# Kernel optimization log

Measured on AMD Instinct MI355X. Metric: run time of the kernel, lower is better.

Reference implementation:

```python
import jax, jax.numpy as jnp
import numpy as np

# ---- problem sizes (would come from edge_index / init args in the torch module) ----
N = 10000      # number of nodes
E = 100000     # number of edges
C = 6          # channels per node
L = 6          # layers
B = 16         # batch
N_IN = 100     # input nodes  (nodes [0, N_IN))
N_OUT = 100    # output nodes (nodes [N-N_OUT, N))
EPS = 1e-5


def setup_inputs() -> dict:
    rng = np.random.default_rng(0)
    src = rng.integers(0, N, size=E).astype(np.int32)
    dst = rng.integers(0, N, size=E).astype(np.int32)

    input_mask = np.zeros(N, bool); input_mask[:N_IN] = True
    output_mask = np.zeros(N, bool); output_mask[N - N_OUT:] = True
    func_mask = ~(input_mask | output_mask)
    func_nodes = np.nonzero(func_mask)[0].astype(np.int32)
    F = func_nodes.size
    ii = np.arange(C, dtype=np.int32)

    # W1 (E -> C*N): edge e feeds all C channels of its dst node. nnz = E*C
    w1_rows = np.repeat(np.arange(E, dtype=np.int32), C)
    w1_cols = (dst[:, None] * C + ii[None, :]).reshape(-1)

    # W2 (C*N -> C*N): dense CxC block per function node. nnz = F*C*C
    base = np.repeat(func_nodes * C, C * C)
    w2_rows = base + np.tile(np.repeat(ii, C), F)
    w2_cols = base + np.tile(np.tile(ii, C), F)

    # W3 (C*N -> E): edge e reads the C channels of src(e) if src is a function node
    e_sel = np.nonzero(func_mask[src])[0].astype(np.int32)
    w3_rows = (src[e_sel][:, None] * C + ii[None, :]).reshape(-1)
    w3_cols = np.repeat(e_sel, C)

    # values: kaiming-style init with fan d (d=C for W1/W2, d=1 for W3)
    w1_vals = (rng.standard_normal(w1_rows.size) / np.sqrt(C)).astype(np.float32)
    w2_vals = (rng.standard_normal(w2_rows.size) / np.sqrt(C)).astype(np.float32)
    w3_vals = (rng.standard_normal(w3_rows.size) * 1.0).astype(np.float32)

    key = jax.random.key(0)
    x = jax.random.normal(key, (B, N), dtype=jnp.float32)

    return {
        "x": x,
        "src": jnp.asarray(src), "dst": jnp.asarray(dst),
        "output_mask": jnp.asarray(output_mask),
        "w1_rows": jnp.asarray(w1_rows), "w1_cols": jnp.asarray(w1_cols),
        "w1_vals": jnp.asarray(w1_vals), "b1": jnp.zeros((C * N,), jnp.float32),
        "w2_rows": jnp.asarray(w2_rows), "w2_cols": jnp.asarray(w2_cols),
        "w2_vals": jnp.asarray(w2_vals), "b2": jnp.zeros((C * N,), jnp.float32),
        "w3_rows": jnp.asarray(w3_rows), "w3_cols": jnp.asarray(w3_cols),
        "w3_vals": jnp.asarray(w3_vals), "b3": jnp.zeros((E,), jnp.float32),
        "gamma": jnp.ones((L,), jnp.float32), "beta": jnp.zeros((L,), jnp.float32),
    }


def _sp_lin(h, rows, cols, vals, bias, out_dim):
    # out[b, c] = sum_{k: cols[k]==c} h[b, rows[k]] * vals[k] + bias[c]
    contrib = h[:, rows] * vals  # [B, nnz]
    out = jnp.zeros((h.shape[0], out_dim), h.dtype).at[:, cols].add(contrib)
    return out + bias


def _batchnorm_scalar(z, g, b):
    # BatchNorm1d(1) on z.view(-1,1): single channel over all B*E elements (training mode)
    m = jnp.mean(z)
    v = jnp.mean(jnp.square(z - m))
    return (z - m) * jax.lax.rsqrt(v + EPS) * g + b


def reference(x, src, dst, output_mask,
              w1_rows, w1_cols, w1_vals, b1,
              w2_rows, w2_cols, w2_vals, b2,
              w3_rows, w3_cols, w3_vals, b3,
              gamma, beta):
    x0 = x[:, src]          # node2edge: [B, E]
    h = x0
    h_last = x0             # residual=True path
    for l in range(L):
        z = _sp_lin(h, w1_rows, w1_cols, w1_vals, b1, C * N)
        z = jax.nn.elu(z)
        z = _sp_lin(z, w2_rows, w2_cols, w2_vals, b2, C * N)
        z = jax.nn.elu(z)
        z = _sp_lin(z, w3_rows, w3_cols, w3_vals, b3, E)
        z = _batchnorm_scalar(z, gamma[l], beta[l])
        h = z + h_last
        h_last = h
    h = h / L
    # edge2node: scatter edge values to dst nodes, keep only output nodes
    node = jnp.zeros((x.shape[0], N), x.dtype).at[:, dst].add(h)
    return jnp.where(output_mask[None, :], node, 0.0)
```

## Files before the change

### kernel.cpp

```cpp
#include <hip/hip_runtime.h>
#include <math.h>

#define NN 10000
#define NE 100000
#define CC 6
#define LL 6
#define BB 16
#define FUNC_LO 100
#define FUNC_HI 9900
#define EPSF 1e-5f
#define NSLOT 64

struct Slot { double s1, s2; double pad[6]; };

struct Params {
  const float *x, *w1v, *b1, *w2v, *b2, *w3v, *b3, *gamma, *beta;
  const int *src, *dst, *w3r, *w3c;
  float *out;
  int *row_start, *counts, *fill, *slot;
  int *row2, *counts2, *fill2, *csr2;
  float4 *grec;
  float4 *srec;
  float *xT, *h, *z3a, *z3b;
  Slot *part, *baseS;
  int F, Ksel;
};

__device__ __forceinline__ float eluf(float x){ return x > 0.0f ? x : expm1f(x); }

__device__ void block_add_slot(double a, double q, Slot* sl){
  __shared__ double sb1[4], sb2[4];
  #pragma unroll
  for(int off=32;off;off>>=1){ a+=__shfl_down(a,off); q+=__shfl_down(q,off); }
  int wid = threadIdx.x>>6;
  if((threadIdx.x&63)==0){ sb1[wid]=a; sb2[wid]=q; }
  __syncthreads();
  if(threadIdx.x==0){
    double A=sb1[0]+sb1[1]+sb1[2]+sb1[3];
    double Q=sb2[0]+sb2[1]+sb2[2]+sb2[3];
    if(A!=0.0) atomicAdd(&sl->s1,A);
    if(Q!=0.0) atomicAdd(&sl->s2,Q);
  }
  __syncthreads();
}

__device__ void bn_params(const Slot* part, const Slot* baseS, float* m, float* inv){
  __shared__ double s_mv[2];
  if(threadIdx.x < NSLOT){
    double a = part[threadIdx.x].s1 + baseS[threadIdx.x].s1;
    double q = part[threadIdx.x].s2 + baseS[threadIdx.x].s2;
    #pragma unroll
    for(int off=32;off;off>>=1){ a+=__shfl_down(a,off); q+=__shfl_down(q,off); }
    if(threadIdx.x==0){
      const double cnt = (double)NE*(double)BB;
      double md = a/cnt, vd = q/cnt - md*md;
      s_mv[0]=md; s_mv[1]=1.0/sqrt(vd+(double)EPSF);
    }
  }
  __syncthreads();
  *m=(float)s_mv[0]; *inv=(float)s_mv[1];
  __syncthreads();
}

__global__ __launch_bounds__(256) void kw_P1(Params p){
  int tid = blockIdx.x*256 + threadIdx.x, nt = gridDim.x*256;
  for(int i=tid;i<NN*BB;i+=nt){ int n=i>>4, b=i&15; p.xT[i]=p.x[b*NN+n]; }
  double a=0.0,q=0.0;
  for(int e=tid;e<NE;e+=nt){
    atomicAdd(&p.counts[p.dst[e]],1);
    int s=p.src[e];
    if(!(s>=FUNC_LO && s<FUNC_HI)){ double v=(double)p.b3[e]; a+=v; q+=v*v; }
  }
  for(int k=tid;k<p.Ksel;k+=nt){
    int s=p.w3r[k*CC]/CC;
    atomicAdd(&p.counts2[s-FUNC_LO],1);
  }
  block_add_slot(a*BB, q*BB, &p.baseS[blockIdx.x&(NSLOT-1)]);
}

__global__ __launch_bounds__(256) void kw_scan(Params p){
  __shared__ int s_scan[256];
  const int*  cin  = (blockIdx.x==0)? p.counts : p.counts2;
  int*        rout = (blockIdx.x==0)? p.row_start : p.row2;
  const int   nel  = (blockIdx.x==0)? NN : p.F;
  const int   CH   = (nel+255)/256;
  int t=threadIdx.x, base=t*CH, s=0;
  for(int k=0;k<CH;k++){ int i=base+k; if(i<nel) s+=cin[i]; }
  s_scan[t]=s; __syncthreads();
  for(int off=1;off<256;off<<=1){
    int v=(t>=off)?s_scan[t-off]:0; __syncthreads();
    s_scan[t]+=v; __syncthreads();
  }
  int run=s_scan[t]-s;
  for(int k=0;k<CH;k++){ int i=base+k; if(i<nel){ rout[i]=run; run+=cin[i]; } }
  if(t==255) rout[nel]=s_scan[255];
}

__global__ __launch_bounds__(256) void kw_fill(Params p){
  int tid = blockIdx.x*256 + threadIdx.x, nt = gridDim.x*256;
  for(int e=tid;e<NE;e+=nt){
    int n=p.dst[e];
    int pos=p.row_start[n]+atomicAdd(&p.fill[n],1);
    p.slot[e]=pos;
    const float* w=&p.w1v[e*CC];
    int s=p.src[e];
    float b3v=p.b3[e];
    p.grec[pos*2  ]=make_float4(w[0],w[1],w[2],w[3]);
    p.grec[pos*2+1]=make_float4(w[4],w[5],__int_as_float(s),b3v);
    if(!(s>=FUNC_LO && s<FUNC_HI)){
      float4 v4=make_float4(b3v,b3v,b3v,b3v);
      float4* za=(float4*)&p.z3a[pos*BB];
      float4* zb=(float4*)&p.z3b[pos*BB];
      #pragma unroll
      for(int i=0;i<4;i++){ za[i]=v4; zb[i]=v4; }
    }
  }
  for(int k=tid;k<p.Ksel;k+=nt){
    int fi=p.w3r[k*CC]/CC - FUNC_LO;
    int pos=p.row2[fi]+atomicAdd(&p.fill2[fi],1);
    p.csr2[pos]=k;
  }
}

template<int MODE>
__global__ __launch_bounds__(256) void kw_AB(Params p, int l,
    const float* __restrict__ z3p, float* __restrict__ z3c){
  int tid = blockIdx.x*256 + (int)threadIdx.x, nt = gridDim.x*256;
  float c1=0.f, c2=0.f;
  if(MODE>0){
    float m, inv;
    bn_params(p.part+(l-1)*NSLOT, p.baseS, &m, &inv);
    float g=p.gamma[l-1], be=p.beta[l-1];
    c1 = inv*g; c2 = be - m*c1;
  }
  const int FB2 = p.F*32;
  double a=0.0, q=0.0;
  for(int t=tid;t<FB2;t+=nt){
    int fi = t>>5;
    int u  = t&31, b = u&15, half = u>>4;
    int n  = FUNC_LO+fi;
    float acc[CC];
    #pragma unroll
    for(int i=0;i<CC;i++) acc[i]=0.f;
    int beg=p.row_start[n], end=p.row_start[n+1];
    int pp = beg + half;
    for(; pp+2<end; pp+=4){
      float4 ra0=p.grec[pp*2],     rb0=p.grec[pp*2+1];
      float4 ra1=p.grec[(pp+2)*2], rb1=p.grec[(pp+2)*2+1];
      float hv0, hv1;
      if(MODE==0){
        int s0=__float_as_int(rb0.z), s1=__float_as_int(rb1.z);
        hv0 = p.xT[s0*BB+b];
        hv1 = p.xT[s1*BB+b];
      } else {
        float zb0=z3p[pp*BB+b], zb1=z3p[(pp+2)*BB+b];
        float hb0, hb1;
        if(MODE==1){
          int s0=__float_as_int(rb0.z), s1=__float_as_int(rb1.z);
          hb0=p.xT[s0*BB+b]; hb1=p.xT[s1*BB+b];
        } else {
          hb0=p.h[pp*BB+b]; hb1=p.h[(pp+2)*BB+b];
        }
        hv0 = hb0 + zb0*c1 + c2;
        hv1 = hb1 + zb1*c1 + c2;
        p.h[pp*BB+b]=hv0; p.h[(pp+2)*BB+b]=hv1;
      }
      acc[0]+=hv0*ra0.x+hv1*ra1.x; acc[1]+=hv0*ra0.y+hv1*ra1.y;
      acc[2]+=hv0*ra0.z+hv1*ra1.z; acc[3]+=hv0*ra0.w+hv1*ra1.w;
      acc[4]+=hv0*rb0.x+hv1*rb1.x; acc[5]+=hv0*rb0.y+hv1*rb1.y;
    }
    if(pp<end){
      float4 ra0=p.grec[pp*2], rb0=p.grec[pp*2+1];
      float hv0;
      if(MODE==0){
        int s0=__float_as_int(rb0.z);
        hv0 = p.xT[s0*BB+b];
      } else {
        float zb0=z3p[pp*BB+b];
        float hb0;
        if(MODE==1){ int s0=__float_as_int(rb0.z); hb0=p.xT[s0*BB+b]; }
        else       { hb0=p.h[pp*BB+b]; }
        hv0 = hb0 + zb0*c1 + c2;
        p.h[pp*BB+b]=hv0;
      }
      acc[0]+=hv0*ra0.x; acc[1]+=hv0*ra0.y; acc[2]+=hv0*ra0.z;
      acc[3]+=hv0*ra0.w; acc[4]+=hv0*rb0.x; acc[5]+=hv0*rb0.y;
    }
    #pragma unroll
    for(int i=0;i<CC;i++){
      acc[i] += __shfl_xor(acc[i],16);
      acc[i]  = eluf(acc[i] + p.b1[n*CC+i]);
    }
    const float* W2=&p.w2v[fi*36];
    float z2[CC];
    #pragma unroll
    for(int jj=0;jj<CC;jj++){
      float o=p.b2[n*CC+jj];
      #pragma unroll
      for(int i=0;i<CC;i++) o+=acc[i]*W2[i*CC+jj];
      z2[jj]=eluf(o);
    }
    int bg2=p.row2[fi], en2=p.row2[fi+1];
    if(MODE==0){
      for(int sp=bg2+half;sp<en2;sp+=2){
        int k=p.csr2[sp];
        int e=p.w3c[k*CC];
        const float* w=&p.w3v[k*CC];
        float b3v=p.b3[e];
        int sl=p.slot[e];
        if(b==0){
          p.srec[sp*2  ]=make_float4(w[0],w[1],w[2],w[3]);
          p.srec[sp*2+1]=make_float4(w[4],w[5],__int_as_float(sl),b3v);
        }
        float o = b3v + z2[0]*w[0]+z2[1]*w[1]+z2[2]*w[2]
                      + z2[3]*w[3]+z2[4]*w[4]+z2[5]*w[5];
        z3c[sl*BB+b]=o;
        a+=o; q+=(double)o*o;
      }
    } else {
      for(int sp=bg2+half;sp<en2;sp+=2){
        float4 ra=p.srec[sp*2], rb=p.srec[sp*2+1];
        float o = rb.w + z2[0]*ra.x + z2[1]*ra.y + z2[2]*ra.z
                       + z2[3]*ra.w + z2[4]*rb.x + z2[5]*rb.y;
        int sl=__float_as_int(rb.z);
        z3c[sl*BB+b]=o;
        a+=o; q+=(double)o*o;
      }
    }
  }
  if(MODE>0){
    int outBeg = p.row_start[FUNC_HI];
    int tot = (p.row_start[NN]-outBeg)*BB;
    for(int u=tid; u<tot; u+=nt){
      int pp=outBeg+(u>>4); int bb=u&15;
      float zb=z3p[pp*BB+bb];
      float hb;
      if(MODE==1){
        float4 rb=p.grec[pp*2+1];
        int s=__float_as_int(rb.z);
        hb=p.xT[s*BB+bb];
      } else {
        hb=p.h[pp*BB+bb];
      }
      p.h[pp*BB+bb]=hb+zb*c1+c2;
    }
  }
  block_add_slot(a,q,&p.part[l*NSLOT+(blockIdx.x&(NSLOT-1))]);
}

__global__ __launch_bounds__(256) void kw_out(Params p, const float* __restrict__ z3p){
  int tid = blockIdx.x*256 + threadIdx.x, nt = gridDim.x*256;
  float m,inv;
  bn_params(p.part+(LL-1)*NSLOT, p.baseS, &m, &inv);
  float g=p.gamma[LL-1], be=p.beta[LL-1];
  float c1=inv*g, c2=be-m*c1;
  for(int idx=tid;idx<BB*NN;idx+=nt){
    int b=idx/NN, n=idx-b*NN;
    float acc=0.f;
    if(n>=FUNC_HI){
      int beg=p.row_start[n], end=p.row_start[n+1];
      for(int pp=beg;pp<end;++pp){
        acc += p.h[pp*BB+b] + z3p[pp*BB+b]*c1 + c2;
      }
      acc *= (1.0f/(float)LL);
    }
    p.out[idx]=acc;
  }
}

extern "C" void kernel_launch(void* const* d_in, const int* in_sizes, int n_in,
                              void* d_out, int out_size, void* d_ws, size_t ws_size,
                              hipStream_t stream){
  Params p;
  p.x    =(const float*)d_in[0];
  p.src  =(const int*)  d_in[1];
  p.dst  =(const int*)  d_in[2];
  p.w1v  =(const float*)d_in[6];
  p.b1   =(const float*)d_in[7];
  p.w2v  =(const float*)d_in[10];
  p.b2   =(const float*)d_in[11];
  p.w3r  =(const int*)  d_in[12];
  p.w3c  =(const int*)  d_in[13];
  p.w3v  =(const float*)d_in[14];
  p.b3   =(const float*)d_in[15];
  p.gamma=(const float*)d_in[16];
  p.beta =(const float*)d_in[17];
  p.out  =(float*)d_out;
  p.F    = in_sizes[8]/36;
  p.Ksel = in_sizes[12]/CC;

  char* ws=(char*)d_ws; size_t off=0;
  auto alloc=[&](size_t bytes)->char*{
    char* q=ws+off; off=(off+bytes+255)&~(size_t)255; return q;
  };
  p.row_start=(int*)   alloc((NN+1)*sizeof(int));
  p.row2     =(int*)   alloc((size_t)(p.F+1)*sizeof(int));
  p.slot     =(int*)   alloc(NE*sizeof(int));
  p.csr2     =(int*)   alloc(NE*sizeof(int));
  p.grec     =(float4*)alloc((size_t)NE*2*sizeof(float4));
  p.srec     =(float4*)alloc((size_t)NE*2*sizeof(float4));
  p.xT       =(float*) alloc((size_t)NN*BB*sizeof(float));
  p.h        =(float*) alloc((size_t)NE*BB*sizeof(float));
  p.z3a      =(float*) alloc((size_t)NE*BB*sizeof(float));
  p.z3b      =(float*) alloc((size_t)NE*BB*sizeof(float));
  p.counts   =(int*)  alloc(NN*sizeof(int));
  p.fill     =(int*)  alloc(NN*sizeof(int));
  p.counts2  =(int*)  alloc((size_t)p.F*sizeof(int));
  p.fill2    =(int*)  alloc((size_t)p.F*sizeof(int));
  p.part     =(Slot*) alloc((size_t)LL*NSLOT*sizeof(Slot));
  p.baseS    =(Slot*) alloc((size_t)NSLOT*sizeof(Slot));
  (void)ws_size; (void)n_in; (void)out_size;

  size_t zspan = (char*)(p.baseS+NSLOT) - (char*)p.counts;
  hipMemsetAsync(p.counts, 0, zspan, stream);

  float* bufs[2] = { p.z3a, p.z3b };
  const int gridAB = (p.F*32 + 255)/256;

  kw_P1  <<<512,256,0,stream>>>(p);
  kw_scan<<<2,  256,0,stream>>>(p);
  kw_fill<<<512,256,0,stream>>>(p);
  kw_AB<0><<<gridAB,256,0,stream>>>(p, 0, bufs[1], bufs[0]);
  kw_AB<1><<<gridAB,256,0,stream>>>(p, 1, bufs[0], bufs[1]);
  for(int l=2;l<LL;l++){
    kw_AB<2><<<gridAB,256,0,stream>>>(p, l, bufs[(l^1)&1], bufs[l&1]);
  }
  kw_out<<<(BB*NN+255)/256,256,0,stream>>>(p, bufs[(LL-1)&1]);
}
```

Baseline: 172.3 us.

## Give each lane four batch columns with float4 loads and shrink output kernel

Each function node's 32 lanes now split as 8 edge sub-streams by 4 float4 batch groups instead of 2 edge halves by 16 scalar batches. Per-edge gathers and stores of xT, h and z3 become 16-byte vector accesses, and the layer-1 reduction gains extra cross-lane shuffle steps. Each lane now keeps six float4 accumulators, which raises register pressure and could lower occupancy. The output kernel only visits the 100 output nodes, and zeroing the rest of the output moves into the first preprocessing kernel.

```diff
diff --git a/kernel.cpp b/kernel.cpp
--- a/kernel.cpp
+++ b/kernel.cpp
@@ -8,6 +8,7 @@
 #define BB 16
 #define FUNC_LO 100
 #define FUNC_HI 9900
+#define NOUT 100
 #define EPSF 1e-5f
 #define NSLOT 64
 
@@ -27,6 +28,12 @@
 };
 
 __device__ __forceinline__ float eluf(float x){ return x > 0.0f ? x : expm1f(x); }
+__device__ __forceinline__ float4 elu4(float4 v){
+  v.x=eluf(v.x); v.y=eluf(v.y); v.z=eluf(v.z); v.w=eluf(v.w); return v;
+}
+__device__ __forceinline__ float4 fma4(float4 a, float s, float4 acc){
+  acc.x+=a.x*s; acc.y+=a.y*s; acc.z+=a.z*s; acc.w+=a.w*s; return acc;
+}
 
 __device__ void block_add_slot(double a, double q, Slot* sl){
   __shared__ double sb1[4], sb2[4];
@@ -65,6 +72,7 @@
 __global__ __launch_bounds__(256) void kw_P1(Params p){
   int tid = blockIdx.x*256 + threadIdx.x, nt = gridDim.x*256;
   for(int i=tid;i<NN*BB;i+=nt){ int n=i>>4, b=i&15; p.xT[i]=p.x[b*NN+n]; }
+  for(int i=tid;i<BB*NN;i+=nt) p.out[i]=0.f;
   double a=0.0,q=0.0;
   for(int e=tid;e<NE;e+=nt){
     atomicAdd(&p.counts[p.dst[e]],1);
@@ -137,112 +145,111 @@
   double a=0.0, q=0.0;
   for(int t=tid;t<FB2;t+=nt){
     int fi = t>>5;
-    int u  = t&31, b = u&15, half = u>>4;
+    int u  = t&31, b4 = u&3, sub = u>>2;
     int n  = FUNC_LO+fi;
-    float acc[CC];
+    float4 acc[CC];
     #pragma unroll
-    for(int i=0;i<CC;i++) acc[i]=0.f;
+    for(int i=0;i<CC;i++) acc[i]=make_float4(0.f,0.f,0.f,0.f);
     int beg=p.row_start[n], end=p.row_start[n+1];
-    int pp = beg + half;
-    for(; pp+2<end; pp+=4){
-      float4 ra0=p.grec[pp*2],     rb0=p.grec[pp*2+1];
-      float4 ra1=p.grec[(pp+2)*2], rb1=p.grec[(pp+2)*2+1];
-      float hv0, hv1;
+    for(int pp=beg+sub; pp<end; pp+=8){
+      float4 ra=p.grec[pp*2], rb=p.grec[pp*2+1];
+      float4 hv;
       if(MODE==0){
-        int s0=__float_as_int(rb0.z), s1=__float_as_int(rb1.z);
-        hv0 = p.xT[s0*BB+b];
-        hv1 = p.xT[s1*BB+b];
+        int s=__float_as_int(rb.z);
+        hv = *(const float4*)&p.xT[s*BB + b4*4];
       } else {
-        float zb0=z3p[pp*BB+b], zb1=z3p[(pp+2)*BB+b];
-        float hb0, hb1;
+        float4 zb = *(const float4*)&z3p[pp*BB + b4*4];
+        float4 hb;
         if(MODE==1){
-          int s0=__float_as_int(rb0.z), s1=__float_as_int(rb1.z);
-          hb0=p.xT[s0*BB+b]; hb1=p.xT[s1*BB+b];
+          int s=__float_as_int(rb.z);
+          hb = *(const float4*)&p.xT[s*BB + b4*4];
         } else {
-          hb0=p.h[pp*BB+b]; hb1=p.h[(pp+2)*BB+b];
+          hb = *(const float4*)&p.h[pp*BB + b4*4];
         }
-        hv0 = hb0 + zb0*c1 + c2;
-        hv1 = hb1 + zb1*c1 + c2;
-        p.h[pp*BB+b]=hv0; p.h[(pp+2)*BB+b]=hv1;
-      }
-      acc[0]+=hv0*ra0.x+hv1*ra1.x; acc[1]+=hv0*ra0.y+hv1*ra1.y;
-      acc[2]+=hv0*ra0.z+hv1*ra1.z; acc[3]+=hv0*ra0.w+hv1*ra1.w;
-      acc[4]+=hv0*rb0.x+hv1*rb1.x; acc[5]+=hv0*rb0.y+hv1*rb1.y;
-    }
-    if(pp<end){
-      float4 ra0=p.grec[pp*2], rb0=p.grec[pp*2+1];
-      float hv0;
-      if(MODE==0){
-        int s0=__float_as_int(rb0.z);
-        hv0 = p.xT[s0*BB+b];
-      } else {
-        float zb0=z3p[pp*BB+b];
-        float hb0;
-        if(MODE==1){ int s0=__float_as_int(rb0.z); hb0=p.xT[s0*BB+b]; }
-        else       { hb0=p.h[pp*BB+b]; }
-        hv0 = hb0 + zb0*c1 + c2;
-        p.h[pp*BB+b]=hv0;
-      }
-      acc[0]+=hv0*ra0.x; acc[1]+=hv0*ra0.y; acc[2]+=hv0*ra0.z;
-      acc[3]+=hv0*ra0.w; acc[4]+=hv0*rb0.x; acc[5]+=hv0*rb0.y;
+        hv.x = hb.x + zb.x*c1 + c2;
+        hv.y = hb.y + zb.y*c1 + c2;
+        hv.z = hb.z + zb.z*c1 + c2;
+        hv.w = hb.w + zb.w*c1 + c2;
+        *(float4*)&p.h[pp*BB + b4*4] = hv;
+      }
+      acc[0]=fma4(hv,ra.x,acc[0]); acc[1]=fma4(hv,ra.y,acc[1]);
+      acc[2]=fma4(hv,ra.z,acc[2]); acc[3]=fma4(hv,ra.w,acc[3]);
+      acc[4]=fma4(hv,rb.x,acc[4]); acc[5]=fma4(hv,rb.y,acc[5]);
     }
     #pragma unroll
     for(int i=0;i<CC;i++){
-      acc[i] += __shfl_xor(acc[i],16);
-      acc[i]  = eluf(acc[i] + p.b1[n*CC+i]);
+      float4 v=acc[i];
+      #pragma unroll
+      for(int mm=4;mm<=16;mm<<=1){
+        v.x += __shfl_xor(v.x,mm);
+        v.y += __shfl_xor(v.y,mm);
+        v.z += __shfl_xor(v.z,mm);
+        v.w += __shfl_xor(v.w,mm);
+      }
+      float b1v=p.b1[n*CC+i];
+      v.x+=b1v; v.y+=b1v; v.z+=b1v; v.w+=b1v;
+      acc[i]=elu4(v);
     }
     const float* W2=&p.w2v[fi*36];
-    float z2[CC];
+    float4 z2[CC];
     #pragma unroll
     for(int jj=0;jj<CC;jj++){
-      float o=p.b2[n*CC+jj];
+      float b2v=p.b2[n*CC+jj];
+      float4 o=make_float4(b2v,b2v,b2v,b2v);
       #pragma unroll
-      for(int i=0;i<CC;i++) o+=acc[i]*W2[i*CC+jj];
-      z2[jj]=eluf(o);
+      for(int i=0;i<CC;i++) o=fma4(acc[i],W2[i*CC+jj],o);
+      z2[jj]=elu4(o);
     }
     int bg2=p.row2[fi], en2=p.row2[fi+1];
     if(MODE==0){
-      for(int sp=bg2+half;sp<en2;sp+=2){
+      for(int sp=bg2+sub;sp<en2;sp+=8){
         int k=p.csr2[sp];
         int e=p.w3c[k*CC];
         const float* w=&p.w3v[k*CC];
         float b3v=p.b3[e];
         int sl=p.slot[e];
-        if(b==0){
+        if(b4==0){
           p.srec[sp*2  ]=make_float4(w[0],w[1],w[2],w[3]);
           p.srec[sp*2+1]=make_float4(w[4],w[5],__int_as_float(sl),b3v);
         }
-        float o = b3v + z2[0]*w[0]+z2[1]*w[1]+z2[2]*w[2]
-                      + z2[3]*w[3]+z2[4]*w[4]+z2[5]*w[5];
-        z3c[sl*BB+b]=o;
-        a+=o; q+=(double)o*o;
+        float4 o=make_float4(b3v,b3v,b3v,b3v);
+        o=fma4(z2[0],w[0],o); o=fma4(z2[1],w[1],o); o=fma4(z2[2],w[2],o);
+        o=fma4(z2[3],w[3],o); o=fma4(z2[4],w[4],o); o=fma4(z2[5],w[5],o);
+        *(float4*)&z3c[sl*BB + b4*4] = o;
+        a+=(double)o.x+o.y+o.z+o.w;
+        q+=(double)o.x*o.x+(double)o.y*o.y+(double)o.z*o.z+(double)o.w*o.w;
       }
     } else {
-      for(int sp=bg2+half;sp<en2;sp+=2){
+      for(int sp=bg2+sub;sp<en2;sp+=8){
         float4 ra=p.srec[sp*2], rb=p.srec[sp*2+1];
-        float o = rb.w + z2[0]*ra.x + z2[1]*ra.y + z2[2]*ra.z
-                       + z2[3]*ra.w + z2[4]*rb.x + z2[5]*rb.y;
+        float4 o=make_float4(rb.w,rb.w,rb.w,rb.w);
+        o=fma4(z2[0],ra.x,o); o=fma4(z2[1],ra.y,o); o=fma4(z2[2],ra.z,o);
+        o=fma4(z2[3],ra.w,o); o=fma4(z2[4],rb.x,o); o=fma4(z2[5],rb.y,o);
         int sl=__float_as_int(rb.z);
-        z3c[sl*BB+b]=o;
-        a+=o; q+=(double)o*o;
+        *(float4*)&z3c[sl*BB + b4*4] = o;
+        a+=(double)o.x+o.y+o.z+o.w;
+        q+=(double)o.x*o.x+(double)o.y*o.y+(double)o.z*o.z+(double)o.w*o.w;
       }
     }
   }
   if(MODE>0){
     int outBeg = p.row_start[FUNC_HI];
-    int tot = (p.row_start[NN]-outBeg)*BB;
+    int tot = (p.row_start[NN]-outBeg)*4;
     for(int u=tid; u<tot; u+=nt){
-      int pp=outBeg+(u>>4); int bb=u&15;
-      float zb=z3p[pp*BB+bb];
-      float hb;
+      int pp=outBeg+(u>>2); int bb4=u&3;
+      float4 zb=*(const float4*)&z3p[pp*BB + bb4*4];
+      float4 hb;
       if(MODE==1){
         float4 rb=p.grec[pp*2+1];
         int s=__float_as_int(rb.z);
-        hb=p.xT[s*BB+bb];
+        hb=*(const float4*)&p.xT[s*BB + bb4*4];
       } else {
-        hb=p.h[pp*BB+bb];
-      }
-      p.h[pp*BB+bb]=hb+zb*c1+c2;
+        hb=*(const float4*)&p.h[pp*BB + bb4*4];
+      }
+      float4 hv;
+      hv.x=hb.x+zb.x*c1+c2; hv.y=hb.y+zb.y*c1+c2;
+      hv.z=hb.z+zb.z*c1+c2; hv.w=hb.w+zb.w*c1+c2;
+      *(float4*)&p.h[pp*BB + bb4*4]=hv;
     }
   }
   block_add_slot(a,q,&p.part[l*NSLOT+(blockIdx.x&(NSLOT-1))]);
@@ -254,17 +261,15 @@
   bn_params(p.part+(LL-1)*NSLOT, p.baseS, &m, &inv);
   float g=p.gamma[LL-1], be=p.beta[LL-1];
   float c1=inv*g, c2=be-m*c1;
-  for(int idx=tid;idx<BB*NN;idx+=nt){
-    int b=idx/NN, n=idx-b*NN;
+  for(int t=tid;t<NOUT*BB;t+=nt){
+    int j=t>>4, b=t&15;
+    int n=FUNC_HI+j;
     float acc=0.f;
-    if(n>=FUNC_HI){
-      int beg=p.row_start[n], end=p.row_start[n+1];
-      for(int pp=beg;pp<end;++pp){
-        acc += p.h[pp*BB+b] + z3p[pp*BB+b]*c1 + c2;
-      }
-      acc *= (1.0f/(float)LL);
-    }
-    p.out[idx]=acc;
+    int beg=p.row_start[n], end=p.row_start[n+1];
+    for(int pp=beg;pp<end;++pp){
+      acc += p.h[pp*BB+b] + z3p[pp*BB+b]*c1 + c2;
+    }
+    p.out[b*NN+n]=acc*(1.0f/(float)LL);
   }
 }
 
@@ -325,5 +330,5 @@
   for(int l=2;l<LL;l++){
     kw_AB<2><<<gridAB,256,0,stream>>>(p, l, bufs[(l^1)&1], bufs[l&1]);
   }
-  kw_out<<<(BB*NN+255)/256,256,0,stream>>>(p, bufs[(LL-1)&1]);
-}
+  kw_out<<<(NOUT*BB+255)/256,256,0,stream>>>(p, bufs[(LL-1)&1]);
+}
```

Result: slower. 178.0 us (+3.3%).

## Update W1 pre-activations incrementally via linearity instead of rebuilding residual h

Applied to the files above, without the earlier changes.

Because the residual update is affine, h_l = h_{l-1} + c1*z3 + c2, the W1 aggregation can be carried forward: A_l = A_{l-1} + c1*(W1·z3) + c2*rowsum(W1). A per-node accumulator A and the W1 row sums are stored in layer 0. Later layers then gather only z3 instead of reading, recomputing and writing h for every incoming edge. The output kernel is also shrunk to launch only over the output nodes, and zeroing of the output moves into the setup kernel. The cost is an extra per-node buffer read and write per layer, plus some floating-point drift from accumulating A across layers.

```diff
diff --git a/kernel.cpp b/kernel.cpp
--- a/kernel.cpp
+++ b/kernel.cpp
@@ -8,6 +8,7 @@
 #define BB 16
 #define FUNC_LO 100
 #define FUNC_HI 9900
+#define NOUT 100
 #define EPSF 1e-5f
 #define NSLOT 64
 
@@ -22,6 +23,8 @@
   float4 *grec;
   float4 *srec;
   float *xT, *h, *z3a, *z3b;
+  float *A;
+  float *Cw;
   Slot *part, *baseS;
   int F, Ksel;
 };
@@ -65,6 +68,7 @@
 __global__ __launch_bounds__(256) void kw_P1(Params p){
   int tid = blockIdx.x*256 + threadIdx.x, nt = gridDim.x*256;
   for(int i=tid;i<NN*BB;i+=nt){ int n=i>>4, b=i&15; p.xT[i]=p.x[b*NN+n]; }
+  for(int i=tid;i<BB*NN;i+=nt) p.out[i]=0.f;
   double a=0.0,q=0.0;
   for(int e=tid;e<NE;e+=nt){
     atomicAdd(&p.counts[p.dst[e]],1);
@@ -139,9 +143,9 @@
     int fi = t>>5;
     int u  = t&31, b = u&15, half = u>>4;
     int n  = FUNC_LO+fi;
-    float acc[CC];
+    float acc[CC], cacc[CC];
     #pragma unroll
-    for(int i=0;i<CC;i++) acc[i]=0.f;
+    for(int i=0;i<CC;i++){ acc[i]=0.f; cacc[i]=0.f; }
     int beg=p.row_start[n], end=p.row_start[n+1];
     int pp = beg + half;
     for(; pp+2<end; pp+=4){
@@ -152,18 +156,11 @@
         int s0=__float_as_int(rb0.z), s1=__float_as_int(rb1.z);
         hv0 = p.xT[s0*BB+b];
         hv1 = p.xT[s1*BB+b];
+        cacc[0]+=ra0.x+ra1.x; cacc[1]+=ra0.y+ra1.y; cacc[2]+=ra0.z+ra1.z;
+        cacc[3]+=ra0.w+ra1.w; cacc[4]+=rb0.x+rb1.x; cacc[5]+=rb0.y+rb1.y;
       } else {
-        float zb0=z3p[pp*BB+b], zb1=z3p[(pp+2)*BB+b];
-        float hb0, hb1;
-        if(MODE==1){
-          int s0=__float_as_int(rb0.z), s1=__float_as_int(rb1.z);
-          hb0=p.xT[s0*BB+b]; hb1=p.xT[s1*BB+b];
-        } else {
-          hb0=p.h[pp*BB+b]; hb1=p.h[(pp+2)*BB+b];
-        }
-        hv0 = hb0 + zb0*c1 + c2;
-        hv1 = hb1 + zb1*c1 + c2;
-        p.h[pp*BB+b]=hv0; p.h[(pp+2)*BB+b]=hv1;
+        hv0 = z3p[pp*BB+b];
+        hv1 = z3p[(pp+2)*BB+b];
       }
       acc[0]+=hv0*ra0.x+hv1*ra1.x; acc[1]+=hv0*ra0.y+hv1*ra1.y;
       acc[2]+=hv0*ra0.z+hv1*ra1.z; acc[3]+=hv0*ra0.w+hv1*ra1.w;
@@ -175,21 +172,32 @@
       if(MODE==0){
         int s0=__float_as_int(rb0.z);
         hv0 = p.xT[s0*BB+b];
+        cacc[0]+=ra0.x; cacc[1]+=ra0.y; cacc[2]+=ra0.z;
+        cacc[3]+=ra0.w; cacc[4]+=rb0.x; cacc[5]+=rb0.y;
       } else {
-        float zb0=z3p[pp*BB+b];
-        float hb0;
-        if(MODE==1){ int s0=__float_as_int(rb0.z); hb0=p.xT[s0*BB+b]; }
-        else       { hb0=p.h[pp*BB+b]; }
-        hv0 = hb0 + zb0*c1 + c2;
-        p.h[pp*BB+b]=hv0;
+        hv0 = z3p[pp*BB+b];
       }
       acc[0]+=hv0*ra0.x; acc[1]+=hv0*ra0.y; acc[2]+=hv0*ra0.z;
       acc[3]+=hv0*ra0.w; acc[4]+=hv0*rb0.x; acc[5]+=hv0*rb0.y;
     }
+    float z1v[CC];
     #pragma unroll
     for(int i=0;i<CC;i++){
       acc[i] += __shfl_xor(acc[i],16);
-      acc[i]  = eluf(acc[i] + p.b1[n*CC+i]);
+      if(MODE==0){
+        cacc[i] += __shfl_xor(cacc[i],16);
+        if(half==0){
+          p.A[(fi*CC+i)*BB+b] = acc[i];
+          if(b==0) p.Cw[fi*CC+i] = cacc[i];
+        }
+        z1v[i] = eluf(acc[i] + p.b1[n*CC+i]);
+      } else {
+        float Aold = p.A[(fi*CC+i)*BB+b];
+        float Cv   = p.Cw[fi*CC+i];
+        float Anew = Aold + c1*acc[i] + c2*Cv;
+        if(half==0) p.A[(fi*CC+i)*BB+b] = Anew;
+        z1v[i] = eluf(Anew + p.b1[n*CC+i]);
+      }
     }
     const float* W2=&p.w2v[fi*36];
     float z2[CC];
@@ -197,7 +205,7 @@
     for(int jj=0;jj<CC;jj++){
       float o=p.b2[n*CC+jj];
       #pragma unroll
-      for(int i=0;i<CC;i++) o+=acc[i]*W2[i*CC+jj];
+      for(int i=0;i<CC;i++) o+=z1v[i]*W2[i*CC+jj];
       z2[jj]=eluf(o);
     }
     int bg2=p.row2[fi], en2=p.row2[fi+1];
@@ -254,17 +262,15 @@
   bn_params(p.part+(LL-1)*NSLOT, p.baseS, &m, &inv);
   float g=p.gamma[LL-1], be=p.beta[LL-1];
   float c1=inv*g, c2=be-m*c1;
-  for(int idx=tid;idx<BB*NN;idx+=nt){
-    int b=idx/NN, n=idx-b*NN;
+  for(int t=tid;t<NOUT*BB;t+=nt){
+    int j=t>>4, b=t&15;
+    int n=FUNC_HI+j;
     float acc=0.f;
-    if(n>=FUNC_HI){
-      int beg=p.row_start[n], end=p.row_start[n+1];
-      for(int pp=beg;pp<end;++pp){
-        acc += p.h[pp*BB+b] + z3p[pp*BB+b]*c1 + c2;
-      }
-      acc *= (1.0f/(float)LL);
-    }
-    p.out[idx]=acc;
+    int beg=p.row_start[n], end=p.row_start[n+1];
+    for(int pp=beg;pp<end;++pp){
+      acc += p.h[pp*BB+b] + z3p[pp*BB+b]*c1 + c2;
+    }
+    p.out[b*NN+n]=acc*(1.0f/(float)LL);
   }
 }
 
@@ -303,6 +309,8 @@
   p.h        =(float*) alloc((size_t)NE*BB*sizeof(float));
   p.z3a      =(float*) alloc((size_t)NE*BB*sizeof(float));
   p.z3b      =(float*) alloc((size_t)NE*BB*sizeof(float));
+  p.A        =(float*) alloc((size_t)p.F*CC*BB*sizeof(float));
+  p.Cw       =(float*) alloc((size_t)p.F*CC*sizeof(float));
   p.counts   =(int*)  alloc(NN*sizeof(int));
   p.fill     =(int*)  alloc(NN*sizeof(int));
   p.counts2  =(int*)  alloc((size_t)p.F*sizeof(int));
@@ -325,5 +333,5 @@
   for(int l=2;l<LL;l++){
     kw_AB<2><<<gridAB,256,0,stream>>>(p, l, bufs[(l^1)&1], bufs[l&1]);
   }
-  kw_out<<<(BB*NN+255)/256,256,0,stream>>>(p, bufs[(LL-1)&1]);
-}
+  kw_out<<<(NOUT*BB+255)/256,256,0,stream>>>(p, bufs[(LL-1)&1]);
+}
```

After: 169.8 us. About the same (-1.5%).
